# Kernel tuning notes

Measured on AMD Instinct MI355X. Metric: run time of the kernel, lower is better.

Reference implementation:

```python
import jax, jax.numpy as jnp
import numpy as np
from jax import lax

_MS_SSIM_WEIGHTS = [0.0448, 0.2856, 0.3001, 0.2363, 0.1333]
LEVELS = 5
WINDOW_SIZE = 11
SIGMA = 1.5
DATA_RANGE = 2.0


def _gaussian_kernel(size, sigma, channels):
    x = jnp.arange(size, dtype=jnp.float32) - size // 2
    g = jnp.exp(-x ** 2 / (2.0 * sigma ** 2))
    g = g / g.sum()
    k2d = jnp.outer(g, g)  # [size, size]
    # depthwise kernel: [C, 1, size, size] (OIHW with feature_group_count=C)
    return jnp.broadcast_to(k2d[None, None], (channels, 1, size, size))


def _depthwise_conv(x, kernel, pad):
    C = x.shape[1]
    return lax.conv_general_dilated(
        x, kernel,
        window_strides=(1, 1),
        padding=[(pad, pad), (pad, pad)],
        dimension_numbers=('NCHW', 'OIHW', 'NCHW'),
        feature_group_count=C)


def _avg_pool2(x):
    s = lax.reduce_window(x, 0.0, lax.add, (1, 1, 2, 2), (1, 1, 2, 2), 'VALID')
    return s * 0.25


def _ssim(x, y, window_size=WINDOW_SIZE, sigma=SIGMA, data_range=DATA_RANGE):
    K1, K2 = 0.01, 0.03
    C1 = (K1 * data_range) ** 2
    C2 = (K2 * data_range) ** 2
    kernel = _gaussian_kernel(window_size, sigma, x.shape[1])
    pad = window_size // 2
    mu1 = _depthwise_conv(x, kernel, pad)
    mu2 = _depthwise_conv(y, kernel, pad)
    mu1_sq = mu1 * mu1
    mu2_sq = mu2 * mu2
    mu1_mu2 = mu1 * mu2
    sig1_sq = _depthwise_conv(x * x, kernel, pad) - mu1_sq
    sig2_sq = _depthwise_conv(y * y, kernel, pad) - mu2_sq
    sig12 = _depthwise_conv(x * y, kernel, pad) - mu1_mu2
    num = (2.0 * mu1_mu2 + C1) * (2.0 * sig12 + C2)
    den = (mu1_sq + mu2_sq + C1) * (sig1_sq + sig2_sq + C2)
    ssim_map = num / (den + 1e-8)
    return ssim_map.mean()


def setup_inputs() -> dict:
    key = jax.random.key(0)
    k1, k2 = jax.random.split(key)
    pred = jax.random.normal(k1, (16, 3, 512, 512), dtype=jnp.float32)
    target = jax.random.normal(k2, (16, 3, 512, 512), dtype=jnp.float32)
    return {"pred": pred, "target": target}


def reference(pred, target):
    weights = jnp.asarray(_MS_SSIM_WEIGHTS[:LEVELS], dtype=jnp.float32)
    weights = weights / weights.sum()
    ms_ssim_val = jnp.zeros((), dtype=jnp.float32)
    x, y = pred, target
    for i in range(LEVELS):
        s = _ssim(x, y)
        ms_ssim_val = ms_ssim_val + weights[i] * s
        if i < LEVELS - 1:
            x = _avg_pool2(x)
            y = _avg_pool2(y)
    return 1.0 - ms_ssim_val
```

## Files before the change

kernel.cpp:

```cpp
#include <hip/hip_runtime.h>


#define NIMG 48
#define NSLOT 256
#define SSTRIDE 16

#define RS1 272
#define RS2 144
#define RS3 80
#define RS4 48
#define IS0 (512L*512)
#define IS1 (256L*272)
#define IS2 (128L*144)
#define IS3 (64L*80)
#define IS4 (32L*48)

typedef float v4f __attribute__((ext_vector_type(4)));
typedef float uf4 __attribute__((ext_vector_type(4), aligned(4)));

struct Pyr { float *x1, *y1, *x2, *y2, *x3, *y3, *x4, *y4; };

#define GDEF const float G[11] = { \
    0.00102839f, 0.00759877f, 0.03600077f, 0.10936069f, 0.21300539f, \
    0.26601173f, 0.21300539f, 0.10936069f, 0.03600077f, 0.00759877f, \
    0.00102839f };

#define WRAP11(v) (((v) + 1 == 11) ? 0 : (v) + 1)

__device__ __forceinline__ void load12(const float* rp, int cb, float* w)
{
#pragma unroll
    for (int v = 0; v < 3; ++v) {
        const uf4 a = *reinterpret_cast<const uf4*>(rp + cb + 4 * v);
        w[4*v+0] = a.x; w[4*v+1] = a.y; w[4*v+2] = a.z; w[4*v+3] = a.w;
    }
}

__device__ __forceinline__ void load12g(const float* rp, int cb, int W, float* w)
{
#pragma unroll
    for (int e = 0; e < 12; ++e) {
        const int col = cb + e;
        w[e] = ((unsigned)col < (unsigned)W) ? rp[col] : 0.0f;
    }
}

__device__ __forceinline__ void l0_win(const float* xi, const float* yi,
                                       int l, int cb, bool edge,
                                       float* xw, float* yw)
{
    if ((unsigned)l < 512u) {
        const float* xr = xi + (long)l * 512;
        const float* yr = yi + (long)l * 512;
        if (!edge) { load12(xr, cb, xw); load12(yr, cb, yw); }
        else       { load12g(xr, cb, 512, xw); load12g(yr, cb, 512, yw); }
    } else {
#pragma unroll
        for (int e = 0; e < 12; ++e) { xw[e] = 0.f; yw[e] = 0.f; }
    }
}

__device__ __forceinline__ void lv_win(const float* xi, const float* yi,
                                       int l, int cb, int H, int rs,
                                       bool laneOK, float* xw, float* yw)
{
    if (((unsigned)l < (unsigned)H) && laneOK) {
        load12(xi + (long)l * rs, cb, xw);
        load12(yi + (long)l * rs, cb, yw);
    } else {
#pragma unroll
        for (int e = 0; e < 12; ++e) { xw[e] = 0.f; yw[e] = 0.f; }
    }
}

__device__ __forceinline__ v4f h_of_row(const float* xw, const float* yw)
{
    GDEF
    v4f s = {0.f, 0.f, 0.f, 0.f};
#pragma unroll
    for (int k = 0; k < 11; ++k) {
        const float a = xw[k], b = yw[k];
        v4f w; w.x = a; w.y = b; w.z = a*a + b*b; w.w = a*b;
        s += w * G[k];
    }
    return s;
}

__device__ __forceinline__ float ssim_px(const v4f acc)
{
    const float C1 = 4.0e-4f;
    const float C2 = 3.6e-3f;
    const float mu1 = acc.x, mu2 = acc.y;
    const float mu1s = mu1*mu1, mu2s = mu2*mu2, m12 = mu1*mu2;
    const float ssum = acc.z - mu1s - mu2s;
    const float s12  = acc.w - m12;
    const float num = (2.f * m12 + C1) * (2.f * s12 + C2);
    const float den = (mu1s + mu2s + C1) * (ssum + C2);
    return num * __builtin_amdgcn_rcpf(den + 1e-8f);
}

__device__ __forceinline__ float vconv(const v4f (*ring)[64], int vb, int lane)
{
    GDEF
    v4f acc = {0.f, 0.f, 0.f, 0.f};
    int sl = vb;
#pragma unroll
    for (int k = 0; k < 11; ++k) {
        acc += ring[sl][lane] * G[k];
        sl = WRAP11(sl);
    }
    return ssim_px(acc);
}

__global__ __launch_bounds__(64, 2) void ssim_l0_stream(
    const float* __restrict__ x, const float* __restrict__ y,
    Pyr p, float* __restrict__ slots)
{
    __shared__ __align__(16) v4f ring[11][64];

    const int lane  = threadIdx.x;
    const int wid   = blockIdx.x;
    const int R0    = (wid & 15) * 32;
    const int strip = (wid >> 4) & 7;
    const int C0    = strip * 64;
    const int z     = wid >> 7;
    const float* xi = x + (long)z * IS0;
    const float* yi = y + (long)z * IS0;
    const bool edge = (strip == 0) | (strip == 7);

    float* q1x = p.x1 + (long)z * IS1;  float* q1y = p.y1 + (long)z * IS1;
    float* q2x = p.x2 + (long)z * IS2;  float* q2y = p.y2 + (long)z * IS2;
    float* q3x = p.x3 + (long)z * IS3;  float* q3y = p.y3 + (long)z * IS3;
    float* q4x = p.x4 + (long)z * IS4;  float* q4y = p.y4 + (long)z * IS4;

    {
        const int r8 = lane >> 3, c8 = lane & 7;
        const int pr0 = R0 + 4 * r8, pc0 = C0 + 8 * c8;
        float v2x0, v2x1, v2y0, v2y1;
        {
            float sx0 = 0.f, sx1 = 0.f, sy0 = 0.f, sy1 = 0.f;
#pragma unroll
            for (int rp = 0; rp < 2; ++rp) {
                const int ir = pr0 + 2 * rp;
                const float* xr = xi + (long)ir * 512 + pc0;
                const float* yr = yi + (long)ir * 512 + pc0;
                const float4 a0 = *reinterpret_cast<const float4*>(xr);
                const float4 a1 = *reinterpret_cast<const float4*>(xr + 4);
                const float4 a2 = *reinterpret_cast<const float4*>(xr + 512);
                const float4 a3 = *reinterpret_cast<const float4*>(xr + 516);
                const float4 b0 = *reinterpret_cast<const float4*>(yr);
                const float4 b1 = *reinterpret_cast<const float4*>(yr + 4);
                const float4 b2 = *reinterpret_cast<const float4*>(yr + 512);
                const float4 b3 = *reinterpret_cast<const float4*>(yr + 516);
                const float qx0 = 0.25f*(a0.x+a0.y+a2.x+a2.y);
                const float qx1 = 0.25f*(a0.z+a0.w+a2.z+a2.w);
                const float qx2 = 0.25f*(a1.x+a1.y+a3.x+a3.y);
                const float qx3 = 0.25f*(a1.z+a1.w+a3.z+a3.w);
                const float qy0 = 0.25f*(b0.x+b0.y+b2.x+b2.y);
                const float qy1 = 0.25f*(b0.z+b0.w+b2.z+b2.w);
                const float qy2 = 0.25f*(b1.x+b1.y+b3.x+b3.y);
                const float qy3 = 0.25f*(b1.z+b1.w+b3.z+b3.w);
                float4 ox; ox.x=qx0; ox.y=qx1; ox.z=qx2; ox.w=qx3;
                float4 oy; oy.x=qy0; oy.y=qy1; oy.z=qy2; oy.w=qy3;
                const int r1 = (R0 >> 1) + 2*r8 + rp;
                *reinterpret_cast<float4*>(q1x + (long)r1*RS1 + (pc0>>1)) = ox;
                *reinterpret_cast<float4*>(q1y + (long)r1*RS1 + (pc0>>1)) = oy;
                sx0 += qx0+qx1; sx1 += qx2+qx3;
                sy0 += qy0+qy1; sy1 += qy2+qy3;
            }
            v2x0 = 0.25f*sx0; v2x1 = 0.25f*sx1;
            v2y0 = 0.25f*sy0; v2y1 = 0.25f*sy1;
            *reinterpret_cast<float2*>(q2x + (long)((R0>>2)+r8)*RS2 + (pc0>>2))
                = make_float2(v2x0, v2x1);
            *reinterpret_cast<float2*>(q2y + (long)((R0>>2)+r8)*RS2 + (pc0>>2))
                = make_float2(v2y0, v2y1);
        }
        const float s3x = v2x0 + v2x1, s3y = v2y0 + v2y1;
        const float v3x = 0.25f*(s3x + __shfl_down(s3x, 8, 64));
        const float v3y = 0.25f*(s3y + __shfl_down(s3y, 8, 64));
        if (!(r8 & 1)) {
            q3x[(long)((R0>>3)+(r8>>1))*RS3 + (C0>>3)+c8] = v3x;
            q3y[(long)((R0>>3)+(r8>>1))*RS3 + (C0>>3)+c8] = v3y;
        }
        const float v4x = 0.25f*(v3x + __shfl_down(v3x,1,64)
                               + __shfl_down(v3x,16,64) + __shfl_down(v3x,17,64));
        const float v4y = 0.25f*(v3y + __shfl_down(v3y,1,64)
                               + __shfl_down(v3y,16,64) + __shfl_down(v3y,17,64));
        if (!(r8 & 3) && !(c8 & 1)) {
            q4x[(long)((R0>>4)+(r8>>2))*RS4 + (C0>>4)+(c8>>1)] = v4x;
            q4y[(long)((R0>>4)+(r8>>2))*RS4 + (C0>>4)+(c8>>1)] = v4y;
        }
        if (edge) {
            const bool left = (strip == 0);
            const int p1c = left ? (c8 - 8) : (256 + c8);
            const int p2c = left ? (c8 - 8) : (128 + c8);
            const int p3c = left ? (c8 - 8) : (64 + c8);
            const int p4c = left ? (c8 - 8) : (32 + c8);
#pragma unroll
            for (int i = 0; i < 2; ++i) {
                const int rr = (R0>>1) + 8*i + r8;
                q1x[(long)rr*RS1 + p1c] = 0.f; q1y[(long)rr*RS1 + p1c] = 0.f;
            }
            { const int rr = (R0>>2) + r8;
              q2x[(long)rr*RS2 + p2c] = 0.f; q2y[(long)rr*RS2 + p2c] = 0.f; }
            if (r8 < 4) {
                const int rr = (R0>>3) + r8;
                q3x[(long)rr*RS3 + p3c] = 0.f; q3y[(long)rr*RS3 + p3c] = 0.f;
            }
            if (r8 < 2) {
                const int rr = (R0>>4) + r8;
                q4x[(long)rr*RS4 + p4c] = 0.f; q4y[(long)rr*RS4 + p4c] = 0.f;
            }
        }
    }
    __builtin_amdgcn_sched_barrier(0);

    const int cb = C0 + lane - 5;
    float local = 0.f;

#pragma unroll 1
    for (int s = 0; s < 10; ++s) {
        float xw[12], yw[12];
        l0_win(xi, yi, R0 - 5 + s, cb, edge, xw, yw);
        ring[s][lane] = h_of_row(xw, yw);
    }

    float xwa[12], ywa[12], xwb[12], ywb[12];
    l0_win(xi, yi, R0 + 5, cb, edge, xwa, ywa);
    int wslot = 10, vb = 0, lload = R0 + 6;
#pragma unroll 1
    for (int pp = 0; pp < 16; ++pp) {
        ring[wslot][lane] = h_of_row(xwa, ywa);
        l0_win(xi, yi, lload, cb, edge, xwb, ywb); ++lload;
        local += vconv(ring, vb, lane);
        wslot = WRAP11(wslot); vb = WRAP11(vb);
        ring[wslot][lane] = h_of_row(xwb, ywb);
        l0_win(xi, yi, lload, cb, edge, xwa, ywa); ++lload;
        local += vconv(ring, vb, lane);
        wslot = WRAP11(wslot); vb = WRAP11(vb);
    }

#pragma unroll
    for (int off = 32; off > 0; off >>= 1) local += __shfl_down(local, off, 64);
    if (lane == 0) atomicAdd(slots + (wid & (NSLOT - 1)) * SSTRIDE, local);
}

__global__ __launch_bounds__(64, 2) void ssim_lvls_stream(
    Pyr p, float* __restrict__ slots)
{
    __shared__ __align__(16) v4f ring[11][64];

    const int lane = threadIdx.x;
    const int wid  = blockIdx.x;

    const float* xi; const float* yi;
    int rs, H, W, C0, R0, lvl;
    if (wid < 1536) {
        lvl = 1; const int r = wid & 31, z = wid >> 5;
        xi = p.x1 + (long)z * IS1; yi = p.y1 + (long)z * IS1;
        rs = RS1; H = W = 256; C0 = (r & 3) * 64; R0 = (r >> 2) * 32;
    } else if (wid < 1920) {
        lvl = 2; const int w2 = wid - 1536; const int r = w2 & 7, z = w2 >> 3;
        xi = p.x2 + (long)z * IS2; yi = p.y2 + (long)z * IS2;
        rs = RS2; H = W = 128; C0 = (r & 1) * 64; R0 = (r >> 1) * 32;
    } else if (wid < 2016) {
        lvl = 3; const int w2 = wid - 1920; const int by = w2 & 1, z = w2 >> 1;
        xi = p.x3 + (long)z * IS3; yi = p.y3 + (long)z * IS3;
        rs = RS3; H = W = 64; C0 = 0; R0 = by * 32;
    } else {
        lvl = 4; const int z = wid - 2016;
        xi = p.x4 + (long)z * IS4; yi = p.y4 + (long)z * IS4;
        rs = RS4; H = W = 32; C0 = 0; R0 = 0;
    }
    const int cb = C0 + lane - 5;
    const bool laneOK = (C0 + lane) < W;
    float local = 0.f;

#pragma unroll 1
    for (int s = 0; s < 10; ++s) {
        float xw[12], yw[12];
        lv_win(xi, yi, R0 - 5 + s, cb, H, rs, laneOK, xw, yw);
        ring[s][lane] = h_of_row(xw, yw);
    }

    float xwa[12], ywa[12], xwb[12], ywb[12];
    lv_win(xi, yi, R0 + 5, cb, H, rs, laneOK, xwa, ywa);
    int wslot = 10, vb = 0, lload = R0 + 6;
#pragma unroll 1
    for (int pp = 0; pp < 16; ++pp) {
        ring[wslot][lane] = h_of_row(xwa, ywa);
        lv_win(xi, yi, lload, cb, H, rs, laneOK, xwb, ywb); ++lload;
        if (laneOK) local += vconv(ring, vb, lane);
        wslot = WRAP11(wslot); vb = WRAP11(vb);
        ring[wslot][lane] = h_of_row(xwb, ywb);
        lv_win(xi, yi, lload, cb, H, rs, laneOK, xwa, ywa); ++lload;
        if (laneOK) local += vconv(ring, vb, lane);
        wslot = WRAP11(wslot); vb = WRAP11(vb);
    }

#pragma unroll
    for (int off = 32; off > 0; off >>= 1) local += __shfl_down(local, off, 64);
    if (lane == 0)
        atomicAdd(slots + ((long)lvl * NSLOT + (wid & (NSLOT - 1))) * SSTRIDE,
                  local);
}

__global__ void finalize_kernel(const float* __restrict__ slots,
                                float* __restrict__ out)
{
    const int t = threadIdx.x;
    const float w[5] = {0.0448f, 0.2856f, 0.3001f, 0.2363f, 0.1333f};
    const float wsum = w[0] + w[1] + w[2] + w[3] + w[4];
    float acc = 0.f;
#pragma unroll
    for (int lvl = 0; lvl < 5; ++lvl) {
        const int d = 512 >> lvl;
        const float cnt = (float)NIMG * (float)d * (float)d;
        acc += (w[lvl] / wsum) / cnt * slots[(lvl * NSLOT + t) * SSTRIDE];
    }
#pragma unroll
    for (int off = 32; off > 0; off >>= 1) acc += __shfl_down(acc, off, 64);
    __shared__ float pp[4];
    if ((t & 63) == 0) pp[t >> 6] = acc;
    __syncthreads();
    if (t == 0) out[0] = 1.0f - (pp[0] + pp[1] + pp[2] + pp[3]);
}

extern "C" void kernel_launch(void* const* d_in, const int* in_sizes, int n_in,
                              void* d_out, int out_size, void* d_ws, size_t ws_size,
                              hipStream_t stream)
{
    const float* pred = (const float*)d_in[0];
    const float* targ = (const float*)d_in[1];
    float* out = (float*)d_out;
    float* ws  = (float*)d_ws;

    float* slots = ws;
    float* zpad  = slots + 5 * NSLOT * SSTRIDE;

    Pyr p;
    {
        float* b = zpad + 640;
        p.x1 = b + 8;                 b += NIMG * IS1;
        p.y1 = b + 8;                 b += NIMG * IS1;
        p.x2 = b + 8;                 b += NIMG * IS2;
        p.y2 = b + 8;                 b += NIMG * IS2;
        p.x3 = b + 8;                 b += NIMG * IS3;
        p.y3 = b + 8;                 b += NIMG * IS3;
        p.x4 = b + 8;                 b += NIMG * IS4;
        p.y4 = b + 8;
    }

    hipMemsetAsync(ws, 0, (size_t)(5 * NSLOT * SSTRIDE + 640) * sizeof(float),
                   stream);

    ssim_l0_stream<<<dim3(6144), 64, 0, stream>>>(pred, targ, p, slots);
    ssim_lvls_stream<<<dim3(2064), 64, 0, stream>>>(p, slots);

    finalize_kernel<<<1, 256, 0, stream>>>(slots, out);
}
```

Before: 273.0 us.

## Pack two waves per block and deepen row prefetch in SSIM streaming kernels

```diff
diff --git a/kernel.cpp b/kernel.cpp
--- a/kernel.cpp
+++ b/kernel.cpp
@@ -99,27 +99,40 @@
     return num * __builtin_amdgcn_rcpf(den + 1e-8f);
 }
 
-__device__ __forceinline__ float vconv(const v4f (*ring)[64], int vb, int lane)
+__device__ __forceinline__ float step_row(v4f (*ring)[64], int vb, int wslot,
+                                          int lane, const float* xw,
+                                          const float* yw)
 {
     GDEF
-    v4f acc = {0.f, 0.f, 0.f, 0.f};
     int sl = vb;
-#pragma unroll
-    for (int k = 0; k < 11; ++k) {
-        acc += ring[sl][lane] * G[k];
-        sl = WRAP11(sl);
-    }
+    const v4f q0 = ring[sl][lane]; sl = WRAP11(sl);
+    const v4f q1 = ring[sl][lane]; sl = WRAP11(sl);
+    const v4f q2 = ring[sl][lane]; sl = WRAP11(sl);
+    const v4f q3 = ring[sl][lane]; sl = WRAP11(sl);
+    const v4f q4 = ring[sl][lane]; sl = WRAP11(sl);
+    const v4f hnew = h_of_row(xw, yw);
+    v4f acc = q0 * G[0];
+    acc += q1 * G[1]; acc += q2 * G[2]; acc += q3 * G[3]; acc += q4 * G[4];
+    const v4f q5 = ring[sl][lane]; sl = WRAP11(sl);
+    const v4f q6 = ring[sl][lane]; sl = WRAP11(sl);
+    const v4f q7 = ring[sl][lane]; sl = WRAP11(sl);
+    const v4f q8 = ring[sl][lane]; sl = WRAP11(sl);
+    const v4f q9 = ring[sl][lane];
+    acc += q5 * G[5]; acc += q6 * G[6]; acc += q7 * G[7]; acc += q8 * G[8];
+    acc += q9 * G[9]; acc += hnew * G[10];
+    ring[wslot][lane] = hnew;
     return ssim_px(acc);
 }
 
-__global__ __launch_bounds__(64, 2) void ssim_l0_stream(
+__global__ __launch_bounds__(128, 2) void ssim_l0_stream(
     const float* __restrict__ x, const float* __restrict__ y,
     Pyr p, float* __restrict__ slots)
 {
-    __shared__ __align__(16) v4f ring[11][64];
-
-    const int lane  = threadIdx.x;
-    const int wid   = blockIdx.x;
+    __shared__ __align__(16) v4f ring[2][11][64];
+
+    const int t     = threadIdx.x;
+    const int lane  = t & 63;
+    const int wid   = blockIdx.x * 2 + (t >> 6);
     const int R0    = (wid & 15) * 32;
     const int strip = (wid >> 4) & 7;
     const int C0    = strip * 64;
@@ -127,6 +140,7 @@
     const float* xi = x + (long)z * IS0;
     const float* yi = y + (long)z * IS0;
     const bool edge = (strip == 0) | (strip == 7);
+    v4f (*myring)[64] = ring[t >> 6];
 
     float* q1x = p.x1 + (long)z * IS1;  float* q1y = p.y1 + (long)z * IS1;
     float* q2x = p.x2 + (long)z * IS2;  float* q2y = p.y2 + (long)z * IS2;
@@ -222,22 +236,21 @@
     for (int s = 0; s < 10; ++s) {
         float xw[12], yw[12];
         l0_win(xi, yi, R0 - 5 + s, cb, edge, xw, yw);
-        ring[s][lane] = h_of_row(xw, yw);
+        myring[s][lane] = h_of_row(xw, yw);
     }
 
     float xwa[12], ywa[12], xwb[12], ywb[12];
     l0_win(xi, yi, R0 + 5, cb, edge, xwa, ywa);
-    int wslot = 10, vb = 0, lload = R0 + 6;
+    l0_win(xi, yi, R0 + 6, cb, edge, xwb, ywb);
+    int wslot = 10, vb = 0, lload = R0 + 7;
 #pragma unroll 1
     for (int pp = 0; pp < 16; ++pp) {
-        ring[wslot][lane] = h_of_row(xwa, ywa);
-        l0_win(xi, yi, lload, cb, edge, xwb, ywb); ++lload;
-        local += vconv(ring, vb, lane);
+        local += step_row(myring, vb, wslot, lane, xwa, ywa);
         wslot = WRAP11(wslot); vb = WRAP11(vb);
-        ring[wslot][lane] = h_of_row(xwb, ywb);
-        l0_win(xi, yi, lload, cb, edge, xwa, ywa); ++lload;
-        local += vconv(ring, vb, lane);
+        if (pp < 15) { l0_win(xi, yi, lload, cb, edge, xwa, ywa); ++lload; }
+        local += step_row(myring, vb, wslot, lane, xwb, ywb);
         wslot = WRAP11(wslot); vb = WRAP11(vb);
+        if (pp < 15) { l0_win(xi, yi, lload, cb, edge, xwb, ywb); ++lload; }
     }
 
 #pragma unroll
@@ -245,13 +258,15 @@
     if (lane == 0) atomicAdd(slots + (wid & (NSLOT - 1)) * SSTRIDE, local);
 }
 
-__global__ __launch_bounds__(64, 2) void ssim_lvls_stream(
+__global__ __launch_bounds__(128, 2) void ssim_lvls_stream(
     Pyr p, float* __restrict__ slots)
 {
-    __shared__ __align__(16) v4f ring[11][64];
-
-    const int lane = threadIdx.x;
-    const int wid  = blockIdx.x;
+    __shared__ __align__(16) v4f ring[2][11][64];
+
+    const int t    = threadIdx.x;
+    const int lane = t & 63;
+    const int wid  = blockIdx.x * 2 + (t >> 6);
+    v4f (*myring)[64] = ring[t >> 6];
 
     const float* xi; const float* yi;
     int rs, H, W, C0, R0, lvl;
@@ -280,22 +295,23 @@
     for (int s = 0; s < 10; ++s) {
         float xw[12], yw[12];
         lv_win(xi, yi, R0 - 5 + s, cb, H, rs, laneOK, xw, yw);
-        ring[s][lane] = h_of_row(xw, yw);
+        myring[s][lane] = h_of_row(xw, yw);
     }
 
     float xwa[12], ywa[12], xwb[12], ywb[12];
     lv_win(xi, yi, R0 + 5, cb, H, rs, laneOK, xwa, ywa);
-    int wslot = 10, vb = 0, lload = R0 + 6;
+    lv_win(xi, yi, R0 + 6, cb, H, rs, laneOK, xwb, ywb);
+    int wslot = 10, vb = 0, lload = R0 + 7;
 #pragma unroll 1
     for (int pp = 0; pp < 16; ++pp) {
-        ring[wslot][lane] = h_of_row(xwa, ywa);
-        lv_win(xi, yi, lload, cb, H, rs, laneOK, xwb, ywb); ++lload;
-        if (laneOK) local += vconv(ring, vb, lane);
+        { const float r = step_row(myring, vb, wslot, lane, xwa, ywa);
+          if (laneOK) local += r; }
         wslot = WRAP11(wslot); vb = WRAP11(vb);
-        ring[wslot][lane] = h_of_row(xwb, ywb);
-        lv_win(xi, yi, lload, cb, H, rs, laneOK, xwa, ywa); ++lload;
-        if (laneOK) local += vconv(ring, vb, lane);
+        if (pp < 15) { lv_win(xi, yi, lload, cb, H, rs, laneOK, xwa, ywa); ++lload; }
+        { const float r = step_row(myring, vb, wslot, lane, xwb, ywb);
+          if (laneOK) local += r; }
         wslot = WRAP11(wslot); vb = WRAP11(vb);
+        if (pp < 15) { lv_win(xi, yi, lload, cb, H, rs, laneOK, xwb, ywb); ++lload; }
     }
 
 #pragma unroll
@@ -354,8 +370,8 @@
     hipMemsetAsync(ws, 0, (size_t)(5 * NSLOT * SSTRIDE + 640) * sizeof(float),
                    stream);
 
-    ssim_l0_stream<<<dim3(6144), 64, 0, stream>>>(pred, targ, p, slots);
-    ssim_lvls_stream<<<dim3(2064), 64, 0, stream>>>(p, slots);
+    ssim_l0_stream<<<dim3(3072), 128, 0, stream>>>(pred, targ, p, slots);
+    ssim_lvls_stream<<<dim3(1032), 128, 0, stream>>>(p, slots);
 
     finalize_kernel<<<1, 256, 0, stream>>>(slots, out);
 }
```

Result: no change. 271.6 us (-0.5%).
